# Kernel tuning notes

Hardware: AMD Instinct MI355X
Metric: run time of the kernel (lower is better)

Reference implementation:

```python
import jax, jax.numpy as jnp
import numpy as np

B, T, C = 2, 4096, 512
H, DH = 8, 64            # num_heads, num_head_channels (per-head dim after reshape)
COND = 512
SCALE = (DH // H) ** -0.5  # faithful to original: (num_head_channels // num_heads)**-0.5


def setup_inputs() -> dict:
    key = jax.random.key(0)
    ks = jax.random.split(key, 6)
    x = jax.random.normal(ks[0], (B, T, C), dtype=jnp.float32)
    condition = jax.random.normal(ks[1], (B, T, COND), dtype=jnp.float32)
    W_qk = jax.random.normal(ks[2], (COND, 2 * H * DH), dtype=jnp.float32) * (COND ** -0.5)
    W_v = jax.random.normal(ks[3], (C, H * DH), dtype=jnp.float32) * (C ** -0.5)
    W_u = jax.random.normal(ks[4], (H * DH, C), dtype=jnp.float32) * ((H * DH) ** -0.5)
    b_u = jax.random.normal(ks[5], (C,), dtype=jnp.float32) * 0.01
    return {"x": x, "condition": condition, "W_qk": W_qk, "W_v": W_v, "W_u": W_u, "b_u": b_u}


def reference(x, condition, W_qk, W_v, W_u, b_u):
    b, t, _ = x.shape
    qk = condition @ W_qk                                  # [b, t, 2*H*DH]
    q, k = jnp.split(qk, 2, axis=-1)
    q = q.reshape(b, t, H, DH).transpose(0, 2, 1, 3)       # [b, H, t, DH]
    k = k.reshape(b, t, H, DH).transpose(0, 2, 1, 3)
    v = (x @ W_v).reshape(b, t, H, DH).transpose(0, 2, 1, 3)
    q = q * SCALE
    dots = jnp.einsum('bhid,bhjd->bhij', q, k)             # [b, H, t, t] (1 GB score matrix)
    attn = jax.nn.softmax(dots, axis=-1)
    out = jnp.einsum('bhij,bhjd->bhid', attn, v)           # [b, H, t, DH]
    out = out.transpose(0, 2, 1, 3).reshape(b, t, H * DH)
    return out @ W_u + b_u
```

## Files before the change

### kernel.cpp

```cpp
#include <hip/hip_runtime.h>

#define B_SZ 2
#define T_SZ 4096

typedef unsigned short u16;
typedef __attribute__((ext_vector_type(8))) short short8;
typedef __attribute__((ext_vector_type(4))) float f32x4;
typedef __attribute__((ext_vector_type(4))) unsigned short u16x4;

#define CEXP 0.51006973f

__device__ __forceinline__ u16 f2bf(float f) {
    unsigned int u;
    __builtin_memcpy(&u, &f, 4);
    u = (u + 0x7fffu + ((u >> 16) & 1u)) >> 16;
    return (u16)u;
}
__device__ __forceinline__ unsigned int rbits(float f) {
    unsigned int u;
    __builtin_memcpy(&u, &f, 4);
    return u + 0x8000u;
}
__device__ __forceinline__ f32x4 mfma16(short8 a, short8 b, f32x4 c) {
    return __builtin_amdgcn_mfma_f32_16x16x32_bf16(a, b, c, 0, 0, 0);
}

__global__ void k_cvt(const float* __restrict__ src, u16* __restrict__ dst) {
    int i = (blockIdx.x * 256 + threadIdx.x) * 4;
    float4 v = *(const float4*)(src + i);
    u16x4 o = { f2bf(v.x), f2bf(v.y), f2bf(v.z), f2bf(v.w) };
    *(u16x4*)(dst + i) = o;
}

__global__ void k_cvt_t(const float* __restrict__ src, u16* __restrict__ dst, int K, int N) {
    int idx = blockIdx.x * 256 + threadIdx.x;
    int k = idx / N, n = idx - k * N;
    dst[(size_t)n * K + k] = f2bf(src[idx]);
}

template <typename OutT, int MODE, int TM, int TN>
__global__ __launch_bounds__(256) void k_gemm2(const u16* __restrict__ A, const u16* __restrict__ Bt,
                                               const float* __restrict__ bias, OutT* __restrict__ C,
                                               OutT* __restrict__ C2, int M, int N) {
    const int K = 512;
    constexpr int MI = TM / 32, NJ = TN / 32;
    constexpr int NA = TM / 64, NB = TN / 64;
    int m0 = blockIdx.x * TM, n0 = blockIdx.y * TN;
    int tid = threadIdx.x;
    int wave = tid >> 6, lane = tid & 63, l16 = lane & 15, q = lane >> 4;
    int mo = (wave & 1) * (TM / 2), no = (wave >> 1) * (TN / 2);

    __shared__ __align__(16) u16 As[TM * 72];
    __shared__ __align__(16) u16 Bs[TN * 72];

    f32x4 acc[MI][NJ];
#pragma unroll
    for (int i = 0; i < MI; ++i)
#pragma unroll
        for (int j = 0; j < NJ; ++j) acc[i][j] = (f32x4){0.f, 0.f, 0.f, 0.f};

    const u16* ap[NA]; const u16* bp[NB];
    short8 ra[NA], rb[NB];
#pragma unroll
    for (int jj = 0; jj < NA; ++jj) {
        int id = tid + 256 * jj;
        ap[jj] = A + (size_t)(m0 + (id >> 2)) * K + (id & 3) * 8;
        ra[jj] = *(const short8*)(ap[jj]);
    }
#pragma unroll
    for (int jj = 0; jj < NB; ++jj) {
        int id = tid + 256 * jj;
        bp[jj] = Bt + (size_t)(n0 + (id >> 2)) * K + (id & 3) * 8;
        rb[jj] = *(const short8*)(bp[jj]);
    }

#pragma unroll 1
    for (int k0 = 0; k0 < K; k0 += 32) {
        __syncthreads();
#pragma unroll
        for (int jj = 0; jj < NA; ++jj) {
            int id = tid + 256 * jj;
            *(short8*)(&As[(id >> 2) * 72 + (id & 3) * 8]) = ra[jj];
        }
#pragma unroll
        for (int jj = 0; jj < NB; ++jj) {
            int id = tid + 256 * jj;
            *(short8*)(&Bs[(id >> 2) * 72 + (id & 3) * 8]) = rb[jj];
        }
        __syncthreads();

        int kadv = (k0 + 32 < K) ? 32 : 0;
#pragma unroll
        for (int jj = 0; jj < NA; ++jj) { ap[jj] += kadv; ra[jj] = *(const short8*)(ap[jj]); }
#pragma unroll
        for (int jj = 0; jj < NB; ++jj) { bp[jj] += kadv; rb[jj] = *(const short8*)(bp[jj]); }
        __builtin_amdgcn_sched_barrier(0);

        short8 af[MI], bf[NJ];
#pragma unroll
        for (int i = 0; i < MI; ++i) af[i] = *(const short8*)(&As[(mo + i * 16 + l16) * 72 + q * 8]);
#pragma unroll
        for (int j = 0; j < NJ; ++j) bf[j] = *(const short8*)(&Bs[(no + j * 16 + l16) * 72 + q * 8]);
#pragma unroll
        for (int i = 0; i < MI; ++i)
#pragma unroll
            for (int j = 0; j < NJ; ++j) acc[i][j] = mfma16(af[i], bf[j], acc[i][j]);
    }

#pragma unroll
    for (int i = 0; i < MI; ++i)
#pragma unroll
        for (int j = 0; j < NJ; ++j)
#pragma unroll
            for (int r = 0; r < 4; ++r) {
                int row = m0 + mo + i * 16 + q * 4 + r;
                int col = n0 + no + j * 16 + l16;
                float val = acc[i][j][r];
                if constexpr (MODE == 0) {
                    val += bias ? bias[col] : 0.f;
                    if constexpr (__is_same(OutT, float)) C[(size_t)row * N + col] = val;
                    else                                  C[(size_t)row * N + col] = f2bf(val);
                } else if constexpr (MODE == 1) {
                    int b = row >> 12, t = row & 4095, h = (col & 511) >> 6, d = col & 63;
                    size_t addr = ((size_t)((b * 8 + h) * 4096 + t)) * 64 + d;
                    if (col < 512) C[addr] = f2bf(val * CEXP);
                    else           C2[addr] = f2bf(val);
                } else {
                    int h = row >> 6, d = row & 63, b = col >> 12, t = col & 4095;
                    int kt = t >> 6, k64 = t & 63;
                    size_t addr = ((((size_t)(b * 8 + h) * 64 + kt) * 64 + d) << 6) + k64;
                    C[addr] = f2bf(val);
                }
            }
}

__global__ __launch_bounds__(256) void k_flash(const u16* __restrict__ Qh, const u16* __restrict__ Kh,
                                               const u16* __restrict__ Vb, u16* __restrict__ o) {
    int qt = blockIdx.x, h = blockIdx.y, b = blockIdx.z;
    int tid = threadIdx.x;
    int wave = tid >> 6, lane = tid & 63, l16 = lane & 15, q = lane >> 4;

    __shared__ __align__(16) u16 Kt[64 * 80];
    __shared__ __align__(16) u16 Vt[64 * 72];

    int head = b * 8 + h;
    const u16* qp = Qh + ((size_t)head * 4096 + qt * 64 + wave * 16 + l16) * 64 + q * 8;
    short8 qf0 = *(const short8*)(qp);
    short8 qf1 = *(const short8*)(qp + 32);

    const u16* kc = Kh + (size_t)head * 4096 * 64;
    const u16* vc = Vb + (size_t)head * 4096 * 64;

    int r0 = tid >> 3, g0 = tid & 7;
    u16* kw0 = &Kt[r0 * 80 + g0 * 8];
    u16* kw1 = &Kt[(r0 + 32) * 80 + g0 * 8];
    u16* vw0 = &Vt[r0 * 72 + g0 * 8];
    u16* vw1 = &Vt[(r0 + 32) * 72 + g0 * 8];

    f32x4 oacc[4];
#pragma unroll
    for (int c = 0; c < 4; ++c) oacc[c] = (f32x4){0.f, 0.f, 0.f, 0.f};
    f32x4 lacc = (f32x4){0.f, 0.f, 0.f, 0.f};
    const short8 ones = { 0x3F80, 0x3F80, 0x3F80, 0x3F80, 0x3F80, 0x3F80, 0x3F80, 0x3F80 };
    int pi0 = (l16 >> 2) * 8 + (l16 & 3);

    short8 rk0 = *(const short8*)(kc + tid * 8);
    short8 rk1 = *(const short8*)(kc + tid * 8 + 2048);
    short8 rv0 = *(const short8*)(vc + tid * 8);
    short8 rv1 = *(const short8*)(vc + tid * 8 + 2048);

#pragma unroll 1
    for (int kt = 0; kt < 64; ++kt) {
        __syncthreads();
        *(short8*)kw0 = rk0;
        *(short8*)kw1 = rk1;
        *(short8*)vw0 = rv0;
        *(short8*)vw1 = rv1;
        __syncthreads();

        int adv = (kt < 63) ? 4096 : 0;
        kc += adv; vc += adv;
        rk0 = *(const short8*)(kc + tid * 8);
        rk1 = *(const short8*)(kc + tid * 8 + 2048);
        rv0 = *(const short8*)(vc + tid * 8);
        rv1 = *(const short8*)(vc + tid * 8 + 2048);
        __builtin_amdgcn_sched_barrier(0);

#pragma unroll
        for (int kk = 0; kk < 2; ++kk) {
            const u16* ka = &Kt[(kk * 32 + pi0) * 80 + q * 8];
            short8 A00 = *(const short8*)(ka);
            short8 A01 = *(const short8*)(ka + 32);
            short8 A10 = *(const short8*)(ka + 4 * 80);
            short8 A11 = *(const short8*)(ka + 4 * 80 + 32);
            f32x4 s0 = (f32x4){0.f, 0.f, 0.f, 0.f};
            f32x4 s1 = (f32x4){0.f, 0.f, 0.f, 0.f};
            s0 = mfma16(A00, qf0, s0); s0 = mfma16(A01, qf1, s0);
            s1 = mfma16(A10, qf0, s1); s1 = mfma16(A11, qf1, s1);

            uint4 pd;
            pd.x = __builtin_amdgcn_perm(rbits(__builtin_amdgcn_exp2f(s0[1])),
                                         rbits(__builtin_amdgcn_exp2f(s0[0])), 0x07060302u);
            pd.y = __builtin_amdgcn_perm(rbits(__builtin_amdgcn_exp2f(s0[3])),
                                         rbits(__builtin_amdgcn_exp2f(s0[2])), 0x07060302u);
            pd.z = __builtin_amdgcn_perm(rbits(__builtin_amdgcn_exp2f(s1[1])),
                                         rbits(__builtin_amdgcn_exp2f(s1[0])), 0x07060302u);
            pd.w = __builtin_amdgcn_perm(rbits(__builtin_amdgcn_exp2f(s1[3])),
                                         rbits(__builtin_amdgcn_exp2f(s1[2])), 0x07060302u);
            short8 pf;
            __builtin_memcpy(&pf, &pd, 16);

            lacc = mfma16(ones, pf, lacc);
#pragma unroll
            for (int c = 0; c < 4; ++c) {
                short8 vfc = *(const short8*)(&Vt[(c * 16 + l16) * 72 + kk * 32 + q * 8]);
                oacc[c] = mfma16(vfc, pf, oacc[c]);
            }
        }
    }

    float inv = 1.f / lacc[0];

    u16* ob = o + (size_t)(b * T_SZ + qt * 64 + wave * 16 + l16) * 512 + h * 64 + q * 4;
#pragma unroll
    for (int c = 0; c < 4; ++c) {
        u16x4 w = { f2bf(oacc[c][0] * inv), f2bf(oacc[c][1] * inv),
                    f2bf(oacc[c][2] * inv), f2bf(oacc[c][3] * inv) };
        *(u16x4*)(ob + c * 16) = w;
    }
}

extern "C" void kernel_launch(void* const* d_in, const int* in_sizes, int n_in,
                              void* d_out, int out_size, void* d_ws, size_t ws_size,
                              hipStream_t stream) {
    const float* x    = (const float*)d_in[0];
    const float* cond = (const float*)d_in[1];
    const float* Wqk  = (const float*)d_in[2];
    const float* Wv   = (const float*)d_in[3];
    const float* Wu   = (const float*)d_in[4];
    const float* bu   = (const float*)d_in[5];
    float* out = (float*)d_out;

    const size_t MT = (size_t)B_SZ * T_SZ;
    u16* xb    = (u16*)d_ws;
    u16* cb    = xb + MT * 512;
    u16* qh_ws = cb + MT * 512;
    u16* kh_ws = qh_ws + MT * 512;
    u16* vb_ws = kh_ws + MT * 512;
    u16* at_ws = vb_ws + MT * 512;
    u16* Wqk_t = at_ws + MT * 512;
    u16* Wv_t  = Wqk_t + (size_t)1024 * 512;
    u16* Wu_t  = Wv_t + (size_t)512 * 512;

    k_cvt<<<(int)(MT * 512 / 1024), 256, 0, stream>>>(x, xb);
    k_cvt<<<(int)(MT * 512 / 1024), 256, 0, stream>>>(cond, cb);
    k_cvt_t<<<(512 * 1024) / 256, 256, 0, stream>>>(Wqk, Wqk_t, 512, 1024);
    k_cvt_t<<<(512 * 512) / 256, 256, 0, stream>>>(Wv, Wv_t, 512, 512);
    k_cvt_t<<<(512 * 512) / 256, 256, 0, stream>>>(Wu, Wu_t, 512, 512);

    k_gemm2<u16, 1, 64, 256><<<dim3(128, 4), 256, 0, stream>>>(cb, Wqk_t, nullptr, qh_ws, kh_ws, 8192, 1024);
    k_gemm2<u16, 2, 128, 64><<<dim3(4, 128), 256, 0, stream>>>(Wv_t, xb, nullptr, vb_ws, nullptr, 512, 8192);
    k_flash<<<dim3(64, 8, 2), 256, 0, stream>>>(qh_ws, kh_ws, vb_ws, at_ws);
    k_gemm2<float, 0, 64, 128><<<dim3(128, 4), 256, 0, stream>>>(at_ws, Wu_t, bu, out, nullptr, 8192, 512);
}
```

Baseline: 244.6 us.

## Merge prep conversions into one kernel and transpose GEMMs for vectorized epilogue stores

```diff
diff --git a/kernel.cpp b/kernel.cpp
--- a/kernel.cpp
+++ b/kernel.cpp
@@ -25,23 +25,34 @@
     return __builtin_amdgcn_mfma_f32_16x16x32_bf16(a, b, c, 0, 0, 0);
 }
 
-__global__ void k_cvt(const float* __restrict__ src, u16* __restrict__ dst) {
-    int i = (blockIdx.x * 256 + threadIdx.x) * 4;
-    float4 v = *(const float4*)(src + i);
-    u16x4 o = { f2bf(v.x), f2bf(v.y), f2bf(v.z), f2bf(v.w) };
-    *(u16x4*)(dst + i) = o;
-}
-
-__global__ void k_cvt_t(const float* __restrict__ src, u16* __restrict__ dst, int K, int N) {
-    int idx = blockIdx.x * 256 + threadIdx.x;
-    int k = idx / N, n = idx - k * N;
-    dst[(size_t)n * K + k] = f2bf(src[idx]);
+__global__ void k_prep(const float* __restrict__ x, const float* __restrict__ cond,
+                       const float* __restrict__ Wqk, const float* __restrict__ Wv,
+                       const float* __restrict__ Wu, u16* __restrict__ xb, u16* __restrict__ cb,
+                       u16* __restrict__ Wqk_t, u16* __restrict__ Wv_t, u16* __restrict__ Wu_t) {
+    int blk = blockIdx.x;
+    if (blk < 8192) {
+        const float* s = blk < 4096 ? x : cond;
+        u16* d = blk < 4096 ? xb : cb;
+        int i = ((blk & 4095) * 256 + threadIdx.x) * 4;
+        float4 v = *(const float4*)(s + i);
+        u16x4 o = { f2bf(v.x), f2bf(v.y), f2bf(v.z), f2bf(v.w) };
+        *(u16x4*)(d + i) = o;
+    } else if (blk < 10240) {
+        int idx = (blk - 8192) * 256 + threadIdx.x;
+        Wqk_t[(size_t)(idx & 1023) * 512 + (idx >> 10)] = f2bf(Wqk[idx]);
+    } else if (blk < 11264) {
+        int idx = (blk - 10240) * 256 + threadIdx.x;
+        Wv_t[(size_t)(idx & 511) * 512 + (idx >> 9)] = f2bf(Wv[idx]);
+    } else {
+        int idx = (blk - 11264) * 256 + threadIdx.x;
+        Wu_t[(size_t)(idx & 511) * 512 + (idx >> 9)] = f2bf(Wu[idx]);
+    }
 }
 
 template <typename OutT, int MODE, int TM, int TN>
-__global__ __launch_bounds__(256) void k_gemm2(const u16* __restrict__ A, const u16* __restrict__ Bt,
+__global__ __launch_bounds__(256) void k_gemm3(const u16* __restrict__ A, const u16* __restrict__ Bt,
                                                const float* __restrict__ bias, OutT* __restrict__ C,
-                                               OutT* __restrict__ C2, int M, int N) {
+                                               OutT* __restrict__ C2) {
     const int K = 512;
     constexpr int MI = TM / 32, NJ = TN / 32;
     constexpr int NA = TM / 64, NB = TN / 64;
@@ -108,30 +119,42 @@
     }
 
 #pragma unroll
-    for (int i = 0; i < MI; ++i)
-#pragma unroll
-        for (int j = 0; j < NJ; ++j)
-#pragma unroll
-            for (int r = 0; r < 4; ++r) {
-                int row = m0 + mo + i * 16 + q * 4 + r;
-                int col = n0 + no + j * 16 + l16;
-                float val = acc[i][j][r];
-                if constexpr (MODE == 0) {
-                    val += bias ? bias[col] : 0.f;
-                    if constexpr (__is_same(OutT, float)) C[(size_t)row * N + col] = val;
-                    else                                  C[(size_t)row * N + col] = f2bf(val);
-                } else if constexpr (MODE == 1) {
-                    int b = row >> 12, t = row & 4095, h = (col & 511) >> 6, d = col & 63;
-                    size_t addr = ((size_t)((b * 8 + h) * 4096 + t)) * 64 + d;
-                    if (col < 512) C[addr] = f2bf(val * CEXP);
-                    else           C2[addr] = f2bf(val);
+    for (int i = 0; i < MI; ++i) {
+        int chb = m0 + mo + i * 16 + q * 4;
+#pragma unroll
+        for (int j = 0; j < NJ; ++j) {
+            int trow = n0 + no + j * 16 + l16;
+            if constexpr (MODE == 0) {
+                float4 bb = *(const float4*)(bias + chb);
+                float4 w = { acc[i][j][0] + bb.x, acc[i][j][1] + bb.y,
+                             acc[i][j][2] + bb.z, acc[i][j][3] + bb.w };
+                *(float4*)(&C[(size_t)trow * 512 + chb]) = w;
+            } else if constexpr (MODE == 1) {
+                int b = trow >> 12, t = trow & 4095;
+                int h = (chb & 511) >> 6, d = chb & 63;
+                size_t addr = ((size_t)((b * 8 + h) * 4096 + t)) * 64 + d;
+                if (chb < 512) {
+                    u16x4 w = { f2bf(acc[i][j][0] * CEXP), f2bf(acc[i][j][1] * CEXP),
+                                f2bf(acc[i][j][2] * CEXP), f2bf(acc[i][j][3] * CEXP) };
+                    *(u16x4*)(&C[addr]) = w;
                 } else {
-                    int h = row >> 6, d = row & 63, b = col >> 12, t = col & 4095;
-                    int kt = t >> 6, k64 = t & 63;
+                    u16x4 w = { f2bf(acc[i][j][0]), f2bf(acc[i][j][1]),
+                                f2bf(acc[i][j][2]), f2bf(acc[i][j][3]) };
+                    *(u16x4*)(&C2[addr]) = w;
+                }
+            } else {
+                int b = trow >> 12, t = trow & 4095;
+                int kt = t >> 6, k64 = t & 63;
+                int h = chb >> 6;
+#pragma unroll
+                for (int r = 0; r < 4; ++r) {
+                    int d = (chb + r) & 63;
                     size_t addr = ((((size_t)(b * 8 + h) * 64 + kt) * 64 + d) << 6) + k64;
-                    C[addr] = f2bf(val);
+                    C[addr] = f2bf(acc[i][j][r]);
                 }
             }
+        }
+    }
 }
 
 __global__ __launch_bounds__(256) void k_flash(const u16* __restrict__ Qh, const u16* __restrict__ Kh,
@@ -252,14 +275,10 @@
     u16* Wv_t  = Wqk_t + (size_t)1024 * 512;
     u16* Wu_t  = Wv_t + (size_t)512 * 512;
 
-    k_cvt<<<(int)(MT * 512 / 1024), 256, 0, stream>>>(x, xb);
-    k_cvt<<<(int)(MT * 512 / 1024), 256, 0, stream>>>(cond, cb);
-    k_cvt_t<<<(512 * 1024) / 256, 256, 0, stream>>>(Wqk, Wqk_t, 512, 1024);
-    k_cvt_t<<<(512 * 512) / 256, 256, 0, stream>>>(Wv, Wv_t, 512, 512);
-    k_cvt_t<<<(512 * 512) / 256, 256, 0, stream>>>(Wu, Wu_t, 512, 512);
-
-    k_gemm2<u16, 1, 64, 256><<<dim3(128, 4), 256, 0, stream>>>(cb, Wqk_t, nullptr, qh_ws, kh_ws, 8192, 1024);
-    k_gemm2<u16, 2, 128, 64><<<dim3(4, 128), 256, 0, stream>>>(Wv_t, xb, nullptr, vb_ws, nullptr, 512, 8192);
+    k_prep<<<12288, 256, 0, stream>>>(x, cond, Wqk, Wv, Wu, xb, cb, Wqk_t, Wv_t, Wu_t);
+
+    k_gemm3<u16, 1, 256, 64><<<dim3(4, 128), 256, 0, stream>>>(Wqk_t, cb, nullptr, qh_ws, kh_ws);
+    k_gemm3<u16, 2, 128, 64><<<dim3(4, 128), 256, 0, stream>>>(Wv_t, xb, nullptr, vb_ws, nullptr);
     k_flash<<<dim3(64, 8, 2), 256, 0, stream>>>(qh_ws, kh_ws, vb_ws, at_ws);
-    k_gemm2<float, 0, 64, 128><<<dim3(128, 4), 256, 0, stream>>>(at_ws, Wu_t, bu, out, nullptr, 8192, 512);
-}
+    k_gemm3<float, 0, 128, 64><<<dim3(4, 128), 256, 0, stream>>>(Wu_t, at_ws, bu, out, nullptr);
+}
```

New measurement: 238.5 us. -2.5%, faster.
